# Optimization experiments

Hardware: AMD Instinct MI355X
Metric: run time of the kernel (lower is better)

The kernel has to match this reference:

```python
import jax, jax.numpy as jnp
import numpy as np

EPS = 1e-5
C = 256
K = 3
K2 = K * K


def conv2d(x, w, b=None, groups=1):
    out = jax.lax.conv_general_dilated(
        x, w, (1, 1), 'VALID',
        dimension_numbers=('NCHW', 'OIHW', 'NCHW'),
        feature_group_count=groups)
    if b is not None:
        out = out + b[None, :, None, None]
    return out


def _bilinear_one(img, py, px):
    # img: [C,H,W]; py,px: [K2,ho,wo] float sampling coords (zero outside)
    _, H, W = img.shape
    y0 = jnp.floor(py)
    x0 = jnp.floor(px)
    dy = py - y0
    dx = px - x0
    y0i = y0.astype(jnp.int32)
    x0i = x0.astype(jnp.int32)

    def gather(yi, xi):
        valid = ((yi >= 0) & (yi < H) & (xi >= 0) & (xi < W)).astype(img.dtype)
        yc = jnp.clip(yi, 0, H - 1)
        xc = jnp.clip(xi, 0, W - 1)
        return img[:, yc, xc] * valid[None]  # [C,K2,ho,wo]

    w00 = (1 - dy) * (1 - dx)
    w01 = (1 - dy) * dx
    w10 = dy * (1 - dx)
    w11 = dy * dx
    return (gather(y0i, x0i) * w00[None] + gather(y0i, x0i + 1) * w01[None]
            + gather(y0i + 1, x0i) * w10[None] + gather(y0i + 1, x0i + 1) * w11[None])


def deform_conv(x, off_w, off_b, w, b):
    # ModulatedDeformConvPack: 3x3, stride=1, pad=0, dil=1, deformable_groups=1
    B, Cin, H, W = x.shape
    ho, wo = H - 2, W - 2
    om = conv2d(x, off_w, off_b)  # [B, 3*K2, ho, wo]
    o1, o2, m = om[:, :K2], om[:, K2:2 * K2], om[:, 2 * K2:]
    offset = jnp.concatenate([o1, o2], axis=1)  # [B, 2*K2, ho, wo]
    off_y = offset[:, 0::2]  # kernel reads y at channel 2k
    off_x = offset[:, 1::2]  # and x at channel 2k+1
    mask = jax.nn.sigmoid(m)  # [B,K2,ho,wo]
    ky, kx = jnp.meshgrid(jnp.arange(K), jnp.arange(K), indexing='ij')
    base_y = (ky.reshape(K2, 1, 1) + jnp.arange(ho).reshape(1, ho, 1)).astype(x.dtype)
    base_x = (kx.reshape(K2, 1, 1) + jnp.arange(wo).reshape(1, 1, wo)).astype(x.dtype)
    py = base_y[None] + off_y
    px = base_x[None] + off_x
    samples = jax.vmap(_bilinear_one)(x, py, px)  # [B,C,K2,ho,wo]
    samples = samples * mask[:, None]
    out = jnp.einsum('bckhw,ock->bohw', samples, w.reshape(w.shape[0], Cin, K2))
    return out + b[None, :, None, None]


def bn(x, g, b_, m, v):
    scale = g / jnp.sqrt(v + EPS)
    return (x - m[None, :, None, None]) * scale[None, :, None, None] + b_[None, :, None, None]


def xcorr(inst, exam):
    # batch-as-groups depthwise cross-correlation
    B = exam.shape[0]
    w = exam.reshape(B * C, 1, 18, 18)
    x = inst.reshape(1, B * C, 30, 30)
    out = jax.lax.conv_general_dilated(
        x, w, (1, 1), 'VALID',
        dimension_numbers=('NCHW', 'OIHW', 'NCHW'),
        feature_group_count=B * C)
    return out.reshape(B, C, 13, 13)


def _forward(examplar, instance, off_w, off_b, dcn_w, dcn_b,
             bn1_g, bn1_b, bn1_m, bn1_v,
             fus_w, fus_b, bn2_g, bn2_b, bn2_m, bn2_v,
             cls_w, cls_b, box_w, box_b):
    def head(x, i):  # deform conv + BN (eval)
        y = deform_conv(x, off_w[i], off_b[i], dcn_w[i], dcn_b[i])
        return bn(y, bn1_g[i], bn1_b[i], bn1_m[i], bn1_v[i])

    exam_cls = head(examplar, 0)
    inst_cls = head(instance, 1)
    exam_reg = head(examplar, 2)
    inst_reg = head(instance, 3)

    xc_cls = xcorr(inst_cls, exam_cls)
    xc_reg = xcorr(inst_reg, exam_reg)

    def fuse(x, i):  # 1x1 conv + BN + ReLU
        y = jnp.einsum('bchw,oc->bohw', x, fus_w[i]) + fus_b[i][None, :, None, None]
        return jax.nn.relu(bn(y, bn2_g[i], bn2_b[i], bn2_m[i], bn2_v[i]))

    f_cls = fuse(xc_cls, 0)
    f_reg = fuse(xc_reg, 1)

    cls_pred = jnp.einsum('bchw,oc->bohw', f_cls, cls_w) + cls_b[None, :, None, None]
    box_pred = jnp.einsum('bchw,oc->bohw', f_reg, box_w) + box_b[None, :, None, None]
    return cls_pred, box_pred


def setup_inputs() -> dict:
    key = jax.random.key(0)
    ks = jax.random.split(key, 24)
    B = 16
    d = {
        'examplar': jax.random.normal(ks[0], (B, C, 20, 20), jnp.float32),
        'instance': jax.random.normal(ks[1], (B, C, 32, 32), jnp.float32),
        # 4 deform heads: 0=exam_cls, 1=inst_cls, 2=exam_reg, 3=inst_reg
        'off_w': jax.random.normal(ks[2], (4, 3 * K2, C, K, K), jnp.float32) * 0.01,
        'off_b': jax.random.normal(ks[3], (4, 3 * K2), jnp.float32) * 0.01,
        'dcn_w': jax.random.normal(ks[4], (4, C, C, K, K), jnp.float32) * 0.05,
        'dcn_b': jax.random.normal(ks[5], (4, C), jnp.float32) * 0.05,
        'bn1_g': jax.random.uniform(ks[6], (4, C), jnp.float32) + 0.5,
        'bn1_b': jax.random.normal(ks[7], (4, C), jnp.float32) * 0.1,
        'bn1_m': jax.random.normal(ks[8], (4, C), jnp.float32) * 0.1,
        'bn1_v': jax.random.uniform(ks[9], (4, C), jnp.float32) + 0.5,
        # 2 fusion modules: 0=cls, 1=reg
        'fus_w': jax.random.normal(ks[10], (2, C, C), jnp.float32) * 0.05,
        'fus_b': jax.random.normal(ks[11], (2, C), jnp.float32) * 0.05,
        'bn2_g': jax.random.uniform(ks[12], (2, C), jnp.float32) + 0.5,
        'bn2_b': jax.random.normal(ks[13], (2, C), jnp.float32) * 0.1,
        'bn2_m': jax.random.normal(ks[14], (2, C), jnp.float32) * 0.1,
        'bn2_v': jax.random.uniform(ks[15], (2, C), jnp.float32) + 0.5,
        'cls_w': jax.random.normal(ks[16], (4, C), jnp.float32) * 0.05,
        'cls_b': jax.random.normal(ks[17], (4,), jnp.float32) * 0.05,
        'box_w': jax.random.normal(ks[18], (16, C), jnp.float32) * 0.05,
        'box_b': jax.random.normal(ks[19], (16,), jnp.float32) * 0.05,
    }
    return d


def reference(examplar, instance, off_w, off_b, dcn_w, dcn_b,
              bn1_g, bn1_b, bn1_m, bn1_v,
              fus_w, fus_b, bn2_g, bn2_b, bn2_m, bn2_v,
              cls_w, cls_b, box_w, box_b):
    return _forward(examplar, instance, off_w, off_b, dcn_w, dcn_b,
                    bn1_g, bn1_b, bn1_m, bn1_v,
                    fus_w, fus_b, bn2_g, bn2_b, bn2_m, bn2_v,
                    cls_w, cls_b, box_w, box_b)
```

## Files before the change

kernel.cpp:

```cpp
#include <hip/hip_runtime.h>
#include <math.h>

#define EPSBN 1e-5f

typedef _Float16 f16x8 __attribute__((ext_vector_type(8)));
typedef _Float16 f16x2 __attribute__((ext_vector_type(2)));
typedef float    f32x4 __attribute__((ext_vector_type(4)));

__device__ __forceinline__ f16x8 splat8(float v) {
  _Float16 h = (_Float16)v;
  return (f16x8){h, h, h, h, h, h, h, h};
}

static constexpr size_t XF_EX = 0;
static constexpr size_t XF_IN = 819200;
static constexpr size_t WPK   = 2916352;
static constexpr size_t OWPK  = 4096000;
static constexpr size_t FWT   = 4243456;
static constexpr size_t OM0   = 4374528;
static constexpr size_t OM1   = 4514496;
static constexpr size_t OM2   = 4903296;
static constexpr size_t OM3   = 5043264;
static constexpr size_t HOUT0 = 5432064;
static constexpr size_t HOUT1 = 6759168;
static constexpr size_t HOUT2 = 10445568;
static constexpr size_t HOUT3 = 11772672;
static constexpr size_t XCB   = 15459072;

__global__ __launch_bounds__(256) void k_transpose(const float* __restrict__ in,
                                                   _Float16* __restrict__ out,
                                                   int H, int W) {
  int y = blockIdx.x, b = blockIdx.y;
  __shared__ float tile[32][257];
  int t = threadIdx.x;
  int x = t & 31, cb = t >> 5;
  for (int c0 = 0; c0 < 256; c0 += 8) {
    int c = c0 + cb;
    if (x < W) tile[x][c] = in[(((size_t)b * 256 + c) * H + y) * W + x];
  }
  __syncthreads();
  for (int x2 = 0; x2 < W; ++x2)
    out[((((size_t)b * H + y) * W + x2) << 8) + t] = (_Float16)tile[x2][t];
}

__global__ __launch_bounds__(256) void k_wpack(const float* __restrict__ w,
                                               _Float16* __restrict__ wp) {
  int idx = blockIdx.x * 256 + threadIdx.x;
  if (idx >= 4 * 9 * 8 * 16 * 64 * 8) return;
  int e  = idx & 7;
  int l  = (idx >> 3) & 63;
  int ot = (idx >> 9) & 15;
  int cs = (idx >> 13) & 7;
  int ht = idx >> 16;
  int tap = ht % 9, h = ht / 9;
  int o = ot * 16 + (l & 15);
  int c = cs * 32 + 8 * (l >> 4) + e;
  wp[idx] = (_Float16)w[((size_t)((h * 256 + o) * 256 + c)) * 9 + tap];
}

__global__ __launch_bounds__(256) void k_owpack(const float* __restrict__ w,
                                                _Float16* __restrict__ wp) {
  int idx = blockIdx.x * 256 + threadIdx.x;
  if (idx >= 4 * 9 * 8 * 2 * 64 * 8) return;
  int e  = idx & 7;
  int l  = (idx >> 3) & 63;
  int ot = (idx >> 9) & 1;
  int cs = (idx >> 10) & 7;
  int ht = idx >> 13;
  int tap = ht % 9, h = ht / 9;
  int o = ot * 16 + (l & 15);
  int c = cs * 32 + 8 * (l >> 4) + e;
  wp[idx] = (o < 27) ? (_Float16)w[((size_t)((h * 27 + o) * 256 + c)) * 9 + tap]
                     : (_Float16)0.f;
}

__global__ __launch_bounds__(256) void k_fwt(const float* __restrict__ w,
                                             float* __restrict__ wt) {
  int idx = blockIdx.x * 256 + threadIdx.x;
  int o = idx & 255, c = (idx >> 8) & 255, i = idx >> 16;
  wt[idx] = w[(i << 16) + (o << 8) + c];
}

__global__ __launch_bounds__(256) void k_offmfma(const _Float16* __restrict__ xh_ex,
                                                 const _Float16* __restrict__ xh_in,
                                                 const _Float16* __restrict__ owpk,
                                                 const float* __restrict__ off_b,
                                                 float* __restrict__ ws) {
  const int h = blockIdx.z, b = blockIdx.y;
  const int HH[4] = {20, 32, 20, 32};
  const size_t OMO[4] = {OM0, OM1, OM2, OM3};
  const int H = HH[h], W = H, ho = H - 2, wo = W - 2, P = ho * wo;
  const int nblk = (P + 63) >> 6;
  if (blockIdx.x >= nblk) return;
  const int p0 = blockIdx.x << 6;
  const _Float16* xh = ((h & 1) ? xh_in : xh_ex) + (((size_t)b * H * W) << 8);

  __shared__ __align__(16) _Float16 S[64 * 256];
  __shared__ int rowoff[64];

  const int t = threadIdx.x, lane = t & 63, wave = t >> 6;
  if (t < 64) {
    int p = min(p0 + t, P - 1);
    int i = p / wo, j = p - i * wo;
    rowoff[t] = (i * W + j) << 8;
  }
  f32x4 acc0 = {0.f, 0.f, 0.f, 0.f}, acc1 = {0.f, 0.f, 0.f, 0.f};
  __syncthreads();

  const int o8 = t & 31;
  for (int tap = 0; tap < 9; ++tap) {
    const int ky = tap / 3, kx = tap - ky * 3;
    const int koff = (ky * W + kx) << 8;
    #pragma unroll
    for (int it = 0; it < 8; ++it) {
      int pl = it * 8 + (t >> 5);
      f16x8 v = *(const f16x8*)(xh + rowoff[pl] + koff + o8 * 8);
      *(f16x8*)((char*)S + pl * 512 + ((o8 * 16) ^ ((pl & 7) << 4))) = v;
    }
    __syncthreads();
    #pragma unroll
    for (int cs = 0; cs < 8; ++cs) {
      int ksg = tap * 8 + cs;
      const _Float16* ab = owpk + ((size_t)(h * 72 + ksg) * 2) * 512 + lane * 8;
      f16x8 a0 = *(const f16x8*)(ab);
      f16x8 a1 = *(const f16x8*)(ab + 512);
      int prow = wave * 16 + (lane & 15);
      f16x8 bf = *(const f16x8*)((char*)S + prow * 512 +
                                 ((cs * 64 + ((lane >> 4) << 4)) ^ ((prow & 7) << 4)));
      acc0 = __builtin_amdgcn_mfma_f32_16x16x32_f16(a0, bf, acc0, 0, 0, 0);
      acc1 = __builtin_amdgcn_mfma_f32_16x16x32_f16(a1, bf, acc1, 0, 0, 0);
    }
    __syncthreads();
  }
  float* om = ws + OMO[h] + (size_t)b * 27 * P;
  int p = p0 + wave * 16 + (lane & 15);
  if (p < P) {
    #pragma unroll
    for (int r = 0; r < 4; ++r) {
      int o = 4 * (lane >> 4) + r;
      if (o < 27) om[o * P + p] = acc0[r] + off_b[h * 27 + o];
      int o2 = o + 16;
      if (o2 < 27) om[o2 * P + p] = acc1[r] + off_b[h * 27 + o2];
    }
  }
}

__global__ __launch_bounds__(256) void k_dgemm(const _Float16* __restrict__ xh_ex,
                                               const _Float16* __restrict__ xh_in,
                                               const _Float16* __restrict__ wpk,
                                               float* __restrict__ ws,
                                               const float* __restrict__ dcn_b,
                                               const float* __restrict__ g1,
                                               const float* __restrict__ b1,
                                               const float* __restrict__ m1,
                                               const float* __restrict__ v1) {
  const int h = blockIdx.z;
  const int HH4[4] = {20, 32, 20, 32};
  const size_t OMO[4] = {OM0, OM1, OM2, OM3};
  const size_t HOO[4] = {HOUT0, HOUT1, HOUT2, HOUT3};
  const int H = HH4[h], W = H, ho = H - 2, wo = W - 2, P = ho * wo;
  const int nblk = (P + 63) >> 6;
  if (blockIdx.x >= nblk) return;
  const int b = blockIdx.y;
  const int p0 = blockIdx.x << 6;
  const _Float16* xh = (h & 1) ? xh_in : xh_ex;
  const float* om = ws + OMO[h] + (size_t)b * 27 * P;
  float* outp = ws + HOO[h] + (size_t)b * 256 * P;

  __shared__ float4 swt4[576];
  __shared__ int4   sad4[576];
  __shared__ __align__(16) _Float16 S[64 * 256];

  const int t = threadIdx.x, lane = t & 63, wave = t >> 6;

  for (int e = t; e < 576; e += 256) {
    int pl = e / 9, k = e - pl * 9;
    float w4[4] = {0.f, 0.f, 0.f, 0.f};
    int a4[4] = {0, 0, 0, 0};
    int p = p0 + pl;
    if (p < P) {
      int i = p / wo, j = p - i * wo;
      float oy = om[(2 * k) * P + p];
      float ox = om[(2 * k + 1) * P + p];
      float mm = om[(18 + k) * P + p];
      float msk = 1.f / (1.f + __expf(-mm));
      int ky = k / 3, kx = k - ky * 3;
      float py = (float)(ky + i) + oy;
      float px = (float)(kx + j) + ox;
      float fy = floorf(py), fx = floorf(px);
      int y0 = (int)fy, x0 = (int)fx;
      float dy = py - fy, dx = px - fx;
      #pragma unroll
      for (int q = 0; q < 4; ++q) {
        int yy = y0 + (q >> 1), xx = x0 + (q & 1);
        bool vld = (yy >= 0) && (yy < H) && (xx >= 0) && (xx < W);
        int yc = min(max(yy, 0), H - 1), xc = min(max(xx, 0), W - 1);
        float wq = ((q >> 1) ? dy : 1.f - dy) * ((q & 1) ? dx : 1.f - dx);
        w4[q] = vld ? wq * msk : 0.f;
        a4[q] = ((blockIdx.y * H + yc) * W + xc) << 8;
      }
    }
    swt4[e] = make_float4(w4[0], w4[1], w4[2], w4[3]);
    sad4[e] = make_int4(a4[0], a4[1], a4[2], a4[3]);
  }

  f32x4 acc[4][4];
  #pragma unroll
  for (int a = 0; a < 4; ++a)
    #pragma unroll
    for (int n = 0; n < 4; ++n) acc[a][n] = (f32x4){0.f, 0.f, 0.f, 0.f};

  __syncthreads();

  const int o8 = t & 31;
  for (int tap = 0; tap < 9; ++tap) {
    #pragma unroll
    for (int it = 0; it < 8; ++it) {
      int pl = it * 8 + (t >> 5);
      float4 w4 = swt4[pl * 9 + tap];
      int4   a4 = sad4[pl * 9 + tap];
      const _Float16* xb = xh + o8 * 8;
      f16x8 x0 = *(const f16x8*)(xb + a4.x);
      f16x8 x1 = *(const f16x8*)(xb + a4.y);
      f16x8 x2 = *(const f16x8*)(xb + a4.z);
      f16x8 x3 = *(const f16x8*)(xb + a4.w);
      f16x8 s = x0 * splat8(w4.x) + x1 * splat8(w4.y) + x2 * splat8(w4.z) + x3 * splat8(w4.w);
      *(f16x8*)((char*)S + pl * 512 + ((o8 * 16) ^ ((pl & 7) << 4))) = s;
    }
    __syncthreads();
    #pragma unroll
    for (int cs = 0; cs < 8; ++cs) {
      int ksg = tap * 8 + cs;
      const _Float16* ab = wpk + ((size_t)(h * 72 + ksg) * 16 + wave * 4) * 512 + lane * 8;
      f16x8 A0 = *(const f16x8*)(ab);
      f16x8 A1 = *(const f16x8*)(ab + 512);
      f16x8 A2 = *(const f16x8*)(ab + 1024);
      f16x8 A3 = *(const f16x8*)(ab + 1536);
      f16x8 B[4];
      #pragma unroll
      for (int n = 0; n < 4; ++n) {
        int prow = n * 16 + (lane & 15);
        B[n] = *(const f16x8*)((char*)S + prow * 512 +
                               ((cs * 64 + ((lane >> 4) << 4)) ^ ((prow & 7) << 4)));
      }
      #pragma unroll
      for (int n = 0; n < 4; ++n) {
        acc[0][n] = __builtin_amdgcn_mfma_f32_16x16x32_f16(A0, B[n], acc[0][n], 0, 0, 0);
        acc[1][n] = __builtin_amdgcn_mfma_f32_16x16x32_f16(A1, B[n], acc[1][n], 0, 0, 0);
        acc[2][n] = __builtin_amdgcn_mfma_f32_16x16x32_f16(A2, B[n], acc[2][n], 0, 0, 0);
        acc[3][n] = __builtin_amdgcn_mfma_f32_16x16x32_f16(A3, B[n], acc[3][n], 0, 0, 0);
      }
    }
    __syncthreads();
  }

  #pragma unroll
  for (int a = 0; a < 4; ++a) {
    int obase = (wave * 4 + a) * 16 + 4 * (lane >> 4);
    #pragma unroll
    for (int r = 0; r < 4; ++r) {
      int o = obase + r;
      float al = g1[h * 256 + o] * rsqrtf(v1[h * 256 + o] + EPSBN);
      float be = (dcn_b[h * 256 + o] - m1[h * 256 + o]) * al + b1[h * 256 + o];
      #pragma unroll
      for (int n = 0; n < 4; ++n) {
        int p = p0 + n * 16 + (lane & 15);
        if (p < P) outp[(size_t)o * P + p] = fmaf(acc[a][n][r], al, be);
      }
    }
  }
}

__global__ __launch_bounds__(256) void k_xcorr3(float* __restrict__ ws) {
  const int br = blockIdx.y;
  const int bc0 = blockIdx.x << 4;
  const float* exg = ws + (br ? HOUT2 : HOUT0) + (size_t)bc0 * 324;
  const float* ing = ws + (br ? HOUT3 : HOUT1) + (size_t)bc0 * 900;
  __shared__ __align__(16) _Float16 exl[16 * 324];
  __shared__ __align__(16) _Float16 inl[16 * 960];
  const int t = threadIdx.x;
  for (int idx = t; idx < 16 * 324; idx += 256)
    exl[idx] = (_Float16)exg[idx];
  for (int idx = t; idx < 16 * 960; idx += 256) {
    int c = idx & 31;
    int rr = idx >> 5;
    inl[idx] = (c < 30) ? (_Float16)ing[rr * 30 + c] : (_Float16)0.f;
  }
  __syncthreads();
  const int lane = t & 63, wave = t >> 6;
  const int sub = lane / 13;
  const int i = lane - sub * 13;
  const bool active = sub < 4;
  const int bcl = wave * 4 + (active ? sub : 0);
  float acc[13];
  #pragma unroll
  for (int j = 0; j < 13; ++j) acc[j] = 0.f;
  const _Float16* inb = inl + bcl * 960;
  const _Float16* exb = exl + bcl * 324;
  for (int u = 0; u < 18; ++u) {
    float a[30];
    const _Float16* rp = inb + (i + u) * 32;
    #pragma unroll
    for (int x = 0; x < 15; ++x) {
      f16x2 pr = *(const f16x2*)(rp + 2 * x);
      a[2 * x] = (float)pr[0]; a[2 * x + 1] = (float)pr[1];
    }
    float e[18];
    const _Float16* ep = exb + u * 18;
    #pragma unroll
    for (int x = 0; x < 9; ++x) {
      f16x2 pr = *(const f16x2*)(ep + 2 * x);
      e[2 * x] = (float)pr[0]; e[2 * x + 1] = (float)pr[1];
    }
    #pragma unroll
    for (int v = 0; v < 18; ++v)
      #pragma unroll
      for (int j = 0; j < 13; ++j)
        acc[j] = fmaf(a[v + j], e[v], acc[j]);
  }
  if (active) {
    float* o = ws + XCB + ((size_t)(br * 4096 + bc0 + bcl)) * 169 + i * 13;
    #pragma unroll
    for (int j = 0; j < 13; ++j) o[j] = acc[j];
  }
}

__global__ __launch_bounds__(256) void k_fuse(float* __restrict__ ws,
                                              const float* __restrict__ fus_b,
                                              const float* __restrict__ g2,
                                              const float* __restrict__ b2,
                                              const float* __restrict__ m2,
                                              const float* __restrict__ v2,
                                              const float* __restrict__ ow,
                                              const float* __restrict__ ob,
                                              float* __restrict__ out,
                                              int n_out, int br) {
  int ij = blockIdx.x, b = blockIdx.y;
  int t = threadIdx.x;
  __shared__ float xv[256];
  __shared__ float fv[256];
  xv[t] = ws[XCB + ((size_t)br * 4096 + b * 256 + t) * 169 + ij];
  __syncthreads();
  const float* fwt = ws + FWT + ((size_t)br << 16);
  float acc = 0.f;
  for (int c = 0; c < 256; ++c) acc = fmaf(fwt[(c << 8) + t], xv[c], acc);
  float s2 = g2[t] * rsqrtf(v2[t] + EPSBN);
  float f = (acc + fus_b[t] - m2[t]) * s2 + b2[t];
  fv[t] = fmaxf(f, 0.f);
  __syncthreads();
  int w = t >> 6, lane = t & 63;
  for (int po = w; po < n_out; po += 4) {
    float part = 0.f;
    #pragma unroll
    for (int q = 0; q < 4; ++q)
      part += ow[(po << 8) + lane + (q << 6)] * fv[lane + (q << 6)];
    for (int off = 32; off; off >>= 1) part += __shfl_down(part, off);
    if (lane == 0) out[((size_t)b * n_out + po) * 169 + ij] = part + ob[po];
  }
}

extern "C" void kernel_launch(void* const* d_in, const int* in_sizes, int n_in,
                              void* d_out, int out_size, void* d_ws, size_t ws_size,
                              hipStream_t stream) {
  const float* ex    = (const float*)d_in[0];
  const float* inst  = (const float*)d_in[1];
  const float* off_w = (const float*)d_in[2];
  const float* off_b = (const float*)d_in[3];
  const float* dcn_w = (const float*)d_in[4];
  const float* dcn_b = (const float*)d_in[5];
  const float* bn1_g = (const float*)d_in[6];
  const float* bn1_b = (const float*)d_in[7];
  const float* bn1_m = (const float*)d_in[8];
  const float* bn1_v = (const float*)d_in[9];
  const float* fus_w = (const float*)d_in[10];
  const float* fus_b = (const float*)d_in[11];
  const float* bn2_g = (const float*)d_in[12];
  const float* bn2_b = (const float*)d_in[13];
  const float* bn2_m = (const float*)d_in[14];
  const float* bn2_v = (const float*)d_in[15];
  const float* cls_w = (const float*)d_in[16];
  const float* cls_b = (const float*)d_in[17];
  const float* box_w = (const float*)d_in[18];
  const float* box_b = (const float*)d_in[19];
  float* out = (float*)d_out;
  float* ws  = (float*)d_ws;

  _Float16* xh_ex = (_Float16*)(ws + XF_EX);
  _Float16* xh_in = (_Float16*)(ws + XF_IN);
  _Float16* wpk   = (_Float16*)(ws + WPK);
  _Float16* owpk  = (_Float16*)(ws + OWPK);

  k_transpose<<<dim3(20, 16), 256, 0, stream>>>(ex,   xh_ex, 20, 20);
  k_transpose<<<dim3(32, 16), 256, 0, stream>>>(inst, xh_in, 32, 32);
  k_wpack <<<9216, 256, 0, stream>>>(dcn_w, wpk);
  k_owpack<<<1152, 256, 0, stream>>>(off_w, owpk);
  k_fwt   <<<512, 256, 0, stream>>>(fus_w, ws + FWT);
  k_offmfma<<<dim3(15, 16, 4), 256, 0, stream>>>(xh_ex, xh_in, owpk, off_b, ws);
  k_dgemm<<<dim3(15, 16, 4), 256, 0, stream>>>(xh_ex, xh_in, wpk, ws,
                                               dcn_b, bn1_g, bn1_b, bn1_m, bn1_v);
  k_xcorr3<<<dim3(256, 2), 256, 0, stream>>>(ws);
  k_fuse<<<dim3(169, 16), 256, 0, stream>>>(ws, fus_b, bn2_g, bn2_b, bn2_m, bn2_v,
                                            cls_w, cls_b, out, 4, 0);
  k_fuse<<<dim3(169, 16), 256, 0, stream>>>(ws, fus_b + 256, bn2_g + 256, bn2_b + 256,
                                            bn2_m + 256, bn2_v + 256, box_w, box_b,
                                            out + 10816, 16, 1);
}
```

Before: 338.1 us.

## Compact tile grids, widen offset/deform GEMM blocks to 512, batch fuse head

The offset-conv and deformable GEMM kernels now use a flattened tile index that maps only to valid tiles across the four heads, which removes idle early-exit blocks. Each block runs 8 waves with fewer accumulators per wave, so each wave does less MFMA work and register pressure drops. The two per-pixel fuse launches are merged into one kernel that handles 13 pixels per block, so each fusion weight load is reused across those pixels. In exchange there are fewer blocks and heavier shared-memory use per block.

```diff
diff --git a/kernel.cpp b/kernel.cpp
--- a/kernel.cpp
+++ b/kernel.cpp
@@ -10,6 +10,13 @@
 __device__ __forceinline__ f16x8 splat8(float v) {
   _Float16 h = (_Float16)v;
   return (f16x8){h, h, h, h, h, h, h, h};
+}
+
+__device__ __forceinline__ void tile_decode(int idx, int& h, int& tl) {
+  if (idx < 6)       { h = 0; tl = idx; }
+  else if (idx < 21) { h = 1; tl = idx - 6; }
+  else if (idx < 27) { h = 2; tl = idx - 21; }
+  else               { h = 3; tl = idx - 27; }
 }
 
 static constexpr size_t XF_EX = 0;
@@ -81,18 +88,18 @@
   wt[idx] = w[(i << 16) + (o << 8) + c];
 }
 
-__global__ __launch_bounds__(256) void k_offmfma(const _Float16* __restrict__ xh_ex,
+__global__ __launch_bounds__(512) void k_offmfma(const _Float16* __restrict__ xh_ex,
                                                  const _Float16* __restrict__ xh_in,
                                                  const _Float16* __restrict__ owpk,
                                                  const float* __restrict__ off_b,
                                                  float* __restrict__ ws) {
-  const int h = blockIdx.z, b = blockIdx.y;
+  int h, tl;
+  tile_decode(blockIdx.x, h, tl);
+  const int b = blockIdx.y;
   const int HH[4] = {20, 32, 20, 32};
   const size_t OMO[4] = {OM0, OM1, OM2, OM3};
   const int H = HH[h], W = H, ho = H - 2, wo = W - 2, P = ho * wo;
-  const int nblk = (P + 63) >> 6;
-  if (blockIdx.x >= nblk) return;
-  const int p0 = blockIdx.x << 6;
+  const int p0 = tl << 6;
   const _Float16* xh = ((h & 1) ? xh_in : xh_ex) + (((size_t)b * H * W) << 8);
 
   __shared__ __align__(16) _Float16 S[64 * 256];
@@ -104,16 +111,18 @@
     int i = p / wo, j = p - i * wo;
     rowoff[t] = (i * W + j) << 8;
   }
-  f32x4 acc0 = {0.f, 0.f, 0.f, 0.f}, acc1 = {0.f, 0.f, 0.f, 0.f};
+  const int ot = wave & 1, nn = wave >> 1;
+  f32x4 acc = {0.f, 0.f, 0.f, 0.f};
   __syncthreads();
 
   const int o8 = t & 31;
+  const int plb = t >> 5;
   for (int tap = 0; tap < 9; ++tap) {
     const int ky = tap / 3, kx = tap - ky * 3;
     const int koff = (ky * W + kx) << 8;
     #pragma unroll
-    for (int it = 0; it < 8; ++it) {
-      int pl = it * 8 + (t >> 5);
+    for (int it = 0; it < 4; ++it) {
+      int pl = it * 16 + plb;
       f16x8 v = *(const f16x8*)(xh + rowoff[pl] + koff + o8 * 8);
       *(f16x8*)((char*)S + pl * 512 + ((o8 * 16) ^ ((pl & 7) << 4))) = v;
     }
@@ -121,31 +130,27 @@
     #pragma unroll
     for (int cs = 0; cs < 8; ++cs) {
       int ksg = tap * 8 + cs;
-      const _Float16* ab = owpk + ((size_t)(h * 72 + ksg) * 2) * 512 + lane * 8;
-      f16x8 a0 = *(const f16x8*)(ab);
-      f16x8 a1 = *(const f16x8*)(ab + 512);
-      int prow = wave * 16 + (lane & 15);
+      const _Float16* ab = owpk + ((size_t)((h * 72 + ksg) * 2 + ot)) * 512 + lane * 8;
+      f16x8 a = *(const f16x8*)(ab);
+      int prow = nn * 16 + (lane & 15);
       f16x8 bf = *(const f16x8*)((char*)S + prow * 512 +
                                  ((cs * 64 + ((lane >> 4) << 4)) ^ ((prow & 7) << 4)));
-      acc0 = __builtin_amdgcn_mfma_f32_16x16x32_f16(a0, bf, acc0, 0, 0, 0);
-      acc1 = __builtin_amdgcn_mfma_f32_16x16x32_f16(a1, bf, acc1, 0, 0, 0);
+      acc = __builtin_amdgcn_mfma_f32_16x16x32_f16(a, bf, acc, 0, 0, 0);
     }
     __syncthreads();
   }
   float* om = ws + OMO[h] + (size_t)b * 27 * P;
-  int p = p0 + wave * 16 + (lane & 15);
+  int p = p0 + nn * 16 + (lane & 15);
   if (p < P) {
     #pragma unroll
     for (int r = 0; r < 4; ++r) {
-      int o = 4 * (lane >> 4) + r;
-      if (o < 27) om[o * P + p] = acc0[r] + off_b[h * 27 + o];
-      int o2 = o + 16;
-      if (o2 < 27) om[o2 * P + p] = acc1[r] + off_b[h * 27 + o2];
-    }
-  }
-}
-
-__global__ __launch_bounds__(256) void k_dgemm(const _Float16* __restrict__ xh_ex,
+      int o = ot * 16 + 4 * (lane >> 4) + r;
+      if (o < 27) om[o * P + p] = acc[r] + off_b[h * 27 + o];
+    }
+  }
+}
+
+__global__ __launch_bounds__(512) void k_dgemm(const _Float16* __restrict__ xh_ex,
                                                const _Float16* __restrict__ xh_in,
                                                const _Float16* __restrict__ wpk,
                                                float* __restrict__ ws,
@@ -154,15 +159,14 @@
                                                const float* __restrict__ b1,
                                                const float* __restrict__ m1,
                                                const float* __restrict__ v1) {
-  const int h = blockIdx.z;
+  int h, tl;
+  tile_decode(blockIdx.x, h, tl);
   const int HH4[4] = {20, 32, 20, 32};
   const size_t OMO[4] = {OM0, OM1, OM2, OM3};
   const size_t HOO[4] = {HOUT0, HOUT1, HOUT2, HOUT3};
   const int H = HH4[h], W = H, ho = H - 2, wo = W - 2, P = ho * wo;
-  const int nblk = (P + 63) >> 6;
-  if (blockIdx.x >= nblk) return;
   const int b = blockIdx.y;
-  const int p0 = blockIdx.x << 6;
+  const int p0 = tl << 6;
   const _Float16* xh = (h & 1) ? xh_in : xh_ex;
   const float* om = ws + OMO[h] + (size_t)b * 27 * P;
   float* outp = ws + HOO[h] + (size_t)b * 256 * P;
@@ -173,7 +177,7 @@
 
   const int t = threadIdx.x, lane = t & 63, wave = t >> 6;
 
-  for (int e = t; e < 576; e += 256) {
+  for (int e = t; e < 576; e += 512) {
     int pl = e / 9, k = e - pl * 9;
     float w4[4] = {0.f, 0.f, 0.f, 0.f};
     int a4[4] = {0, 0, 0, 0};
@@ -197,26 +201,27 @@
         int yc = min(max(yy, 0), H - 1), xc = min(max(xx, 0), W - 1);
         float wq = ((q >> 1) ? dy : 1.f - dy) * ((q & 1) ? dx : 1.f - dx);
         w4[q] = vld ? wq * msk : 0.f;
-        a4[q] = ((blockIdx.y * H + yc) * W + xc) << 8;
+        a4[q] = ((b * H + yc) * W + xc) << 8;
       }
     }
     swt4[e] = make_float4(w4[0], w4[1], w4[2], w4[3]);
     sad4[e] = make_int4(a4[0], a4[1], a4[2], a4[3]);
   }
 
-  f32x4 acc[4][4];
+  f32x4 acc[2][4];
   #pragma unroll
-  for (int a = 0; a < 4; ++a)
+  for (int a = 0; a < 2; ++a)
     #pragma unroll
     for (int n = 0; n < 4; ++n) acc[a][n] = (f32x4){0.f, 0.f, 0.f, 0.f};
 
   __syncthreads();
 
   const int o8 = t & 31;
+  const int plb = t >> 5;
   for (int tap = 0; tap < 9; ++tap) {
     #pragma unroll
-    for (int it = 0; it < 8; ++it) {
-      int pl = it * 8 + (t >> 5);
+    for (int it = 0; it < 4; ++it) {
+      int pl = it * 16 + plb;
       float4 w4 = swt4[pl * 9 + tap];
       int4   a4 = sad4[pl * 9 + tap];
       const _Float16* xb = xh + o8 * 8;
@@ -231,11 +236,9 @@
     #pragma unroll
     for (int cs = 0; cs < 8; ++cs) {
       int ksg = tap * 8 + cs;
-      const _Float16* ab = wpk + ((size_t)(h * 72 + ksg) * 16 + wave * 4) * 512 + lane * 8;
+      const _Float16* ab = wpk + ((size_t)(h * 72 + ksg) * 16 + wave * 2) * 512 + lane * 8;
       f16x8 A0 = *(const f16x8*)(ab);
       f16x8 A1 = *(const f16x8*)(ab + 512);
-      f16x8 A2 = *(const f16x8*)(ab + 1024);
-      f16x8 A3 = *(const f16x8*)(ab + 1536);
       f16x8 B[4];
       #pragma unroll
       for (int n = 0; n < 4; ++n) {
@@ -247,16 +250,14 @@
       for (int n = 0; n < 4; ++n) {
         acc[0][n] = __builtin_amdgcn_mfma_f32_16x16x32_f16(A0, B[n], acc[0][n], 0, 0, 0);
         acc[1][n] = __builtin_amdgcn_mfma_f32_16x16x32_f16(A1, B[n], acc[1][n], 0, 0, 0);
-        acc[2][n] = __builtin_amdgcn_mfma_f32_16x16x32_f16(A2, B[n], acc[2][n], 0, 0, 0);
-        acc[3][n] = __builtin_amdgcn_mfma_f32_16x16x32_f16(A3, B[n], acc[3][n], 0, 0, 0);
       }
     }
     __syncthreads();
   }
 
   #pragma unroll
-  for (int a = 0; a < 4; ++a) {
-    int obase = (wave * 4 + a) * 16 + 4 * (lane >> 4);
+  for (int a = 0; a < 2; ++a) {
+    int obase = (wave * 2 + a) * 16 + 4 * (lane >> 4);
     #pragma unroll
     for (int r = 0; r < 4; ++r) {
       int o = obase + r;
@@ -325,37 +326,63 @@
   }
 }
 
-__global__ __launch_bounds__(256) void k_fuse(float* __restrict__ ws,
-                                              const float* __restrict__ fus_b,
-                                              const float* __restrict__ g2,
-                                              const float* __restrict__ b2,
-                                              const float* __restrict__ m2,
-                                              const float* __restrict__ v2,
-                                              const float* __restrict__ ow,
-                                              const float* __restrict__ ob,
-                                              float* __restrict__ out,
-                                              int n_out, int br) {
-  int ij = blockIdx.x, b = blockIdx.y;
-  int t = threadIdx.x;
-  __shared__ float xv[256];
-  __shared__ float fv[256];
-  xv[t] = ws[XCB + ((size_t)br * 4096 + b * 256 + t) * 169 + ij];
-  __syncthreads();
-  const float* fwt = ws + FWT + ((size_t)br << 16);
-  float acc = 0.f;
-  for (int c = 0; c < 256; ++c) acc = fmaf(fwt[(c << 8) + t], xv[c], acc);
-  float s2 = g2[t] * rsqrtf(v2[t] + EPSBN);
-  float f = (acc + fus_b[t] - m2[t]) * s2 + b2[t];
-  fv[t] = fmaxf(f, 0.f);
-  __syncthreads();
-  int w = t >> 6, lane = t & 63;
-  for (int po = w; po < n_out; po += 4) {
+__global__ __launch_bounds__(256) void k_fuse2(float* __restrict__ ws,
+                                               const float* __restrict__ fus_b,
+                                               const float* __restrict__ g2,
+                                               const float* __restrict__ b2,
+                                               const float* __restrict__ m2,
+                                               const float* __restrict__ v2,
+                                               const float* __restrict__ cls_w,
+                                               const float* __restrict__ cls_b,
+                                               const float* __restrict__ box_w,
+                                               const float* __restrict__ box_b,
+                                               float* __restrict__ out) {
+  const int ij0 = blockIdx.x * 13;
+  const int b = blockIdx.y;
+  const int br = blockIdx.z;
+  const int n_out = br ? 16 : 4;
+  const float* ow = br ? box_w : cls_w;
+  const float* ob = br ? box_b : cls_b;
+  float* outp = out + (br ? (size_t)10816 : 0);
+
+  __shared__ float xv[256 * 13];
+  __shared__ float fv[13 * 257];
+  const int t = threadIdx.x;
+  const float* src = ws + XCB + ((size_t)br * 4096 + b * 256) * 169;
+  for (int idx = t; idx < 256 * 13; idx += 256) {
+    int c = idx / 13, j = idx - c * 13;
+    xv[idx] = src[(size_t)c * 169 + ij0 + j];
+  }
+  __syncthreads();
+
+  const float* fwt = ws + FWT + ((size_t)br << 16) + t;
+  float acc[13];
+  #pragma unroll
+  for (int j = 0; j < 13; ++j) acc[j] = 0.f;
+  for (int c = 0; c < 256; ++c) {
+    float wv = fwt[c << 8];
+    #pragma unroll
+    for (int j = 0; j < 13; ++j)
+      acc[j] = fmaf(wv, xv[c * 13 + j], acc[j]);
+  }
+  float s2 = g2[br * 256 + t] * rsqrtf(v2[br * 256 + t] + EPSBN);
+  float fb = fus_b[br * 256 + t], mm = m2[br * 256 + t], bb = b2[br * 256 + t];
+  #pragma unroll
+  for (int j = 0; j < 13; ++j)
+    fv[j * 257 + t] = fmaxf((acc[j] + fb - mm) * s2 + bb, 0.f);
+  __syncthreads();
+
+  const int g = t >> 4, l16 = t & 15;
+  for (int wi = g; wi < 13 * n_out; wi += 16) {
+    int j = wi / n_out, po = wi - j * n_out;
     float part = 0.f;
     #pragma unroll
-    for (int q = 0; q < 4; ++q)
-      part += ow[(po << 8) + lane + (q << 6)] * fv[lane + (q << 6)];
-    for (int off = 32; off; off >>= 1) part += __shfl_down(part, off);
-    if (lane == 0) out[((size_t)b * n_out + po) * 169 + ij] = part + ob[po];
+    for (int q = 0; q < 16; ++q)
+      part = fmaf(ow[(po << 8) + l16 + (q << 4)], fv[j * 257 + l16 + (q << 4)], part);
+    #pragma unroll
+    for (int off = 8; off; off >>= 1) part += __shfl_xor(part, off);
+    if (l16 == 0)
+      outp[((size_t)b * n_out + po) * 169 + ij0 + j] = part + ob[po];
   }
 }
 
@@ -395,13 +422,10 @@
   k_wpack <<<9216, 256, 0, stream>>>(dcn_w, wpk);
   k_owpack<<<1152, 256, 0, stream>>>(off_w, owpk);
   k_fwt   <<<512, 256, 0, stream>>>(fus_w, ws + FWT);
-  k_offmfma<<<dim3(15, 16, 4), 256, 0, stream>>>(xh_ex, xh_in, owpk, off_b, ws);
-  k_dgemm<<<dim3(15, 16, 4), 256, 0, stream>>>(xh_ex, xh_in, wpk, ws,
-                                               dcn_b, bn1_g, bn1_b, bn1_m, bn1_v);
+  k_offmfma<<<dim3(42, 16), 512, 0, stream>>>(xh_ex, xh_in, owpk, off_b, ws);
+  k_dgemm<<<dim3(42, 16), 512, 0, stream>>>(xh_ex, xh_in, wpk, ws,
+                                            dcn_b, bn1_g, bn1_b, bn1_m, bn1_v);
   k_xcorr3<<<dim3(256, 2), 256, 0, stream>>>(ws);
-  k_fuse<<<dim3(169, 16), 256, 0, stream>>>(ws, fus_b, bn2_g, bn2_b, bn2_m, bn2_v,
-                                            cls_w, cls_b, out, 4, 0);
-  k_fuse<<<dim3(169, 16), 256, 0, stream>>>(ws, fus_b + 256, bn2_g + 256, bn2_b + 256,
-                                            bn2_m + 256, bn2_v + 256, box_w, box_b,
-                                            out + 10816, 16, 1);
-}
+  k_fuse2<<<dim3(13, 16, 2), 256, 0, stream>>>(ws, fus_b, bn2_g, bn2_b, bn2_m, bn2_v,
+                                               cls_w, cls_b, box_w, box_b, out);
+}
```

After: 330.1 us. -2.3%, faster.
